# Kernel optimization log

Hardware: AMD Instinct MI355X
Metric: run time of the kernel (lower is better)

## Reference

```python
import jax, jax.numpy as jnp
import numpy as np

N_SPLIT = 4      # n_splits=[4]
RED_FC = 32      # reduce_fc
OUT_NC = 32      # reduce_adc
K = 3            # adc kernel
FMN1, FMN2 = 2048, 2048


def _adaptive_avg_matrix(in_size, out_size):
    # PyTorch AdaptiveAvgPool2d window rule: start=floor(i*in/out), end=ceil((i+1)*in/out)
    M = np.zeros((out_size, in_size), np.float32)
    for i in range(out_size):
        s = (i * in_size) // out_size
        e = -((-(i + 1) * in_size) // out_size)
        M[i, s:e] = 1.0 / (e - s)
    return jnp.asarray(M)


def grid_slice(x, n_split):
    # x: (B,C,H,W); H,W divisible by n_split (xh_padding==0). Pad 1, take overlapping tiles.
    B, C, H, W = x.shape
    hs, ws = H // n_split, W // n_split
    xp = jnp.pad(x, ((0, 0), (0, 0), (1, 1), (1, 1)))
    tiles = [xp[:, :, i * hs:i * hs + hs + 2, j * ws:j * ws + ws + 2]
             for i in range(n_split) for j in range(n_split)]
    return jnp.stack(tiles, axis=1)  # (B, n^2, C, hs+2, ws+2)


def grid_splice(x, n_split):
    # x: (B, n^2, C, hs, ws) tiles in row-major (hh, ww) order -> (B, C, H, W)
    B, T, C, hs, ws = x.shape
    x = x.reshape(B, n_split, n_split, C, hs, ws)
    x = x.transpose(0, 3, 1, 4, 2, 5)
    return x.reshape(B, C, n_split * hs, n_split * ws)


def conv2d(x, w, b, padding):
    y = jax.lax.conv_general_dilated(x, w, (1, 1), padding,
                                     dimension_numbers=("NCHW", "OIHW", "NCHW"))
    return y + b[None, :, None, None]


def setup_inputs() -> dict:
    key = jax.random.key(0)
    ks = jax.random.split(key, 8)
    B, C, H, W = 4, 64, 256, 256
    fc_size = RED_FC * RED_FC                    # 1024
    wsize = OUT_NC * C * K * K                   # 18432
    f32 = jnp.float32
    return {
        "feature": jax.random.normal(ks[0], (B, C, H, W), f32),
        # reducer: Conv(C->C,3,p1) + LeakyReLU(0.2) + Conv(C->1,3,p1) + Tanh
        "rw1": jax.random.normal(ks[1], (C, C, 3, 3), f32) * 0.05,
        "rb1": jnp.zeros((C,), f32),
        "rw2": jax.random.normal(ks[2], (1, C, 3, 3), f32) * 0.05,
        "rb2": jnp.zeros((1,), f32),
        # filter-manifold network: fc_size -> 2048 -> 2048 -> (weights + bias)
        "fw1": jax.random.normal(ks[3], (fc_size, FMN1), f32) * 0.02,
        "fb1": jnp.zeros((FMN1,), f32),
        "fw2": jax.random.normal(ks[4], (FMN1, FMN2), f32) * 0.02,
        "fb2": jnp.zeros((FMN2,), f32),
        "fw3": jax.random.normal(ks[5], (FMN2, wsize + OUT_NC), f32) * 0.01,
        "fb3": jnp.zeros((wsize + OUT_NC,), f32),
    }


def reference(feature, rw1, rb1, rw2, rb2, fw1, fb1, fw2, fb2, fw3, fb3):
    B, C, H, W = feature.shape
    # reducer -> 1-channel adaptive map
    h = conv2d(feature, rw1, rb1, ((1, 1), (1, 1)))
    h = jnp.where(h >= 0, h, 0.2 * h)                       # LeakyReLU(0.2)
    adaptive = jnp.tanh(conv2d(h, rw2, rb2, ((1, 1), (1, 1))))  # (B,1,H,W)

    # per-region context gram via adaptive avg pool to (32,32)
    adap = grid_slice(adaptive, N_SPLIT)                    # (B,T,1,hs+2,ws+2)
    Bt, T, ac, ah, aw = adap.shape
    Mh = _adaptive_avg_matrix(ah, RED_FC)
    Mw = _adaptive_avg_matrix(aw, RED_FC)
    gram = jnp.einsum("ph,btchw,qw->btcpq", Mh, adap, Mw).reshape(B * T, -1)  # (B*T,1024)

    # FMN generates per-(batch,tile) conv weights + bias
    g = jax.nn.relu(gram @ fw1 + fb1)
    g = jax.nn.relu(g @ fw2 + fb2)
    wb = g @ fw3 + fb3                                      # (B*T, wsize+OUT_NC)
    wsize = OUT_NC * C * K * K
    dyn_w = wb[:, :wsize].reshape(B * T * OUT_NC, C, K, K)
    dyn_b = wb[:, wsize:]                                   # (B*T, OUT_NC)

    # dynamic-weight VALID conv per tile via grouped conv
    fea = grid_slice(feature, N_SPLIT)                      # (B,T,C,hs+2,ws+2)
    fh, fw_ = fea.shape[-2], fea.shape[-1]
    x = fea.reshape(1, B * T * C, fh, fw_)
    y = jax.lax.conv_general_dilated(x, dyn_w, (1, 1), "VALID",
                                     dimension_numbers=("NCHW", "OIHW", "NCHW"),
                                     feature_group_count=B * T)
    y = y.reshape(B * T, OUT_NC, fh - 2, fw_ - 2) + dyn_b[:, :, None, None]
    y = grid_splice(y.reshape(B, T, OUT_NC, fh - 2, fw_ - 2), N_SPLIT)  # (B,32,H,W)

    # short_cut=True, training path: concat along channels
    return jnp.concatenate([feature, y], axis=1)            # (B, C+32, H, W)
```

## Files before the change

### kernel.cpp

```cpp
#include <hip/hip_runtime.h>


__global__ __launch_bounds__(256) void transp_rw1_k(
    const float* __restrict__ rw1, float* __restrict__ rt)
{
    int idx = blockIdx.x * 256 + threadIdx.x;
    if (idx >= 36864) return;
    int ocg = idx / 9216;
    int r   = idx - ocg * 9216;
    int ic  = r / 144;
    int r2  = r - ic * 144;
    int k   = r2 >> 4;
    int o   = r2 & 15;
    rt[idx] = rw1[(((size_t)(ocg * 16 + o) * 64 + ic) * 9) + k];
}

template <int MODE>
__global__ __launch_bounds__(256, 3) void conv3x3_v2(
    const float* __restrict__ in,
    const float* __restrict__ wt,
    const float* __restrict__ bbf,
    float* __restrict__ outb)
{
    __shared__ float sIn[8 * 34 * 36];

    const int bx = blockIdx.x, by = blockIdx.y, bz = blockIdx.z;
    int b, ocg;
    if (MODE == 0) { b = bz >> 2; ocg = bz & 3; }
    else           { b = bz >> 1; ocg = bz & 1; }
    const int tid = threadIdx.x;
    const int tx = tid & 15, ty = tid >> 4;
    const int x0 = bx * 32, y0 = by * 32;

    int bt = 0;
    const float* wbase;
    if (MODE == 0) {
        wbase = wt + ocg * 9216;
    } else {
        bt = b * 16 + (by >> 1) * 4 + (bx >> 1);
        wbase = wt + (size_t)bt * 18464 + ocg * 9216;
    }

    float acc[2][2][16];
#pragma unroll
    for (int rg = 0; rg < 2; ++rg)
#pragma unroll
        for (int p = 0; p < 2; ++p)
#pragma unroll
            for (int oc = 0; oc < 16; ++oc) acc[rg][p][oc] = 0.f;

    for (int cc = 0; cc < 8; ++cc) {
        __syncthreads();
        for (int idx = tid; idx < 8 * 34 * 34; idx += 256) {
            int ic  = idx / 1156;
            int rem = idx - ic * 1156;
            int r   = rem / 34;
            int c   = rem - r * 34;
            int gy = y0 + r - 1, gx = x0 + c - 1;
            float v = 0.f;
            if ((unsigned)gy < 256u && (unsigned)gx < 256u)
                v = in[(((size_t)b * 64 + cc * 8 + ic) * 256 + gy) * 256 + gx];
            sIn[ic * 1224 + r * 36 + c] = v;
        }
        __syncthreads();

        const float* wc = wbase + cc * 8 * 144;
        for (int ic = 0; ic < 8; ++ic) {
            const float* sI = &sIn[ic * 1224 + ty * 36 + 2 * tx];
            const float* wp = wc + ic * 144;
#pragma unroll
            for (int kh = 0; kh < 3; ++kh) {
                float w[3][16];
#pragma unroll
                for (int kw = 0; kw < 3; ++kw) {
                    *(float4*)&w[kw][0]  = *(const float4*)&wp[(kh * 3 + kw) * 16 + 0];
                    *(float4*)&w[kw][4]  = *(const float4*)&wp[(kh * 3 + kw) * 16 + 4];
                    *(float4*)&w[kw][8]  = *(const float4*)&wp[(kh * 3 + kw) * 16 + 8];
                    *(float4*)&w[kw][12] = *(const float4*)&wp[(kh * 3 + kw) * 16 + 12];
                }
#pragma unroll
                for (int rg = 0; rg < 2; ++rg) {
                    const float* rp = sI + (rg * 16 + kh) * 36;
                    float2 a  = *(const float2*)&rp[0];
                    float2 bq = *(const float2*)&rp[2];
                    float iv[4] = {a.x, a.y, bq.x, bq.y};
#pragma unroll
                    for (int kw = 0; kw < 3; ++kw) {
#pragma unroll
                        for (int oc = 0; oc < 16; ++oc) {
                            acc[rg][0][oc] += iv[kw]     * w[kw][oc];
                            acc[rg][1][oc] += iv[kw + 1] * w[kw][oc];
                        }
                    }
                }
            }
        }
    }

#pragma unroll
    for (int rg = 0; rg < 2; ++rg) {
        const int gy = y0 + ty + rg * 16;
#pragma unroll
        for (int oc = 0; oc < 16; ++oc) {
            float bv;
            int plane;
            if (MODE == 0) {
                bv = bbf[ocg * 16 + oc];
                plane = b * 96 + ocg * 16 + oc;
            } else {
                bv = bbf[(size_t)bt * 18464 + 18432 + ocg * 16 + oc];
                plane = b * 96 + 64 + ocg * 16 + oc;
            }
            float v0 = acc[rg][0][oc] + bv;
            float v1 = acc[rg][1][oc] + bv;
            if (MODE == 0) {
                v0 = (v0 >= 0.f) ? v0 : 0.2f * v0;
                v1 = (v1 >= 0.f) ? v1 : 0.2f * v1;
            }
            size_t o = (((size_t)plane) * 256 + gy) * 256 + x0 + 2 * tx;
            float2 st = {v0, v1};
            *(float2*)&outb[o] = st;
        }
    }
}

__global__ __launch_bounds__(256) void conv2_tanh_k(
    const float* __restrict__ hin,
    const float* __restrict__ rw2,
    const float* __restrict__ rb2,
    float* __restrict__ ad)
{
    __shared__ float sIn[16 * 18 * 35];
    __shared__ float sW[144];
    const int bx = blockIdx.x, by = blockIdx.y, b = blockIdx.z;
    const int tid = threadIdx.x;
    const int tx = tid & 15, ty = tid >> 4;
    const int x0 = bx * 32, y0 = by * 16;
    float a0 = 0.f, a1 = 0.f;

    for (int cc = 0; cc < 4; ++cc) {
        __syncthreads();
        for (int idx = tid; idx < 16 * 18 * 34; idx += 256) {
            int ic = idx / 612;
            int rem = idx - ic * 612;
            int row = rem / 34;
            int col = rem - row * 34;
            int gy = y0 + row - 1, gx = x0 + col - 1;
            float v = 0.f;
            if ((unsigned)gy < 256u && (unsigned)gx < 256u)
                v = hin[(((size_t)b * 96 + cc * 16 + ic) * 256 + gy) * 256 + gx];
            sIn[ic * 630 + row * 35 + col] = v;
        }
        if (tid < 144) sW[tid] = rw2[cc * 144 + tid];
        __syncthreads();

        for (int ic = 0; ic < 16; ++ic) {
            const float* sI = &sIn[ic * 630 + ty * 35 + tx];
            const float* sWi = &sW[ic * 9];
#pragma unroll
            for (int k = 0; k < 9; ++k) {
                const int kh = k / 3, kw = k - kh * 3;
                float w = sWi[k];
                a0 += sI[kh * 35 + kw] * w;
                a1 += sI[kh * 35 + kw + 16] * w;
            }
        }
    }
    float bias = rb2[0];
    size_t o = ((size_t)b * 256 + y0 + ty) * 256 + x0 + tx;
    ad[o] = tanhf(a0 + bias);
    ad[o + 16] = tanhf(a1 + bias);
}

__global__ __launch_bounds__(256) void gram_pool_k(
    const float* __restrict__ adaptive, float* __restrict__ gram)
{
    int idx = blockIdx.x * 256 + threadIdx.x;
    int bt = idx >> 10;
    int pq = idx & 1023;
    int p = pq >> 5, q = pq & 31;
    int b = bt >> 4, t = bt & 15;
    int ti = t >> 2, tj = t & 3;
    int sp = (p * 33) >> 4, ep = ((p + 1) * 33 + 15) >> 4;
    int sq = (q * 33) >> 4, eq = ((q + 1) * 33 + 15) >> 4;
    float s = 0.f;
    for (int hh = sp; hh < ep; ++hh) {
        int gy = ti * 64 + hh - 1;
        if ((unsigned)gy >= 256u) continue;
        for (int w = sq; w < eq; ++w) {
            int gx = tj * 64 + w - 1;
            if ((unsigned)gx < 256u) s += adaptive[((size_t)b * 256 + gy) * 256 + gx];
        }
    }
    gram[idx] = s / (float)((ep - sp) * (eq - sq));
}

__global__ __launch_bounds__(256) void fc_gemm_k(
    const float* __restrict__ A, const float* __restrict__ Bm,
    const float* __restrict__ bias, float* __restrict__ Cm,
    int K, int N, int act, int trans)
{
    __shared__ float As[16][68];
    __shared__ float Bs[16][64];
    const int n0 = blockIdx.x * 64;
    const int tid = threadIdx.x;
    const int tx = tid & 15, ty = tid >> 4;
    float acc[4][4];
#pragma unroll
    for (int i = 0; i < 4; ++i)
#pragma unroll
        for (int j = 0; j < 4; ++j) acc[i][j] = 0.f;

    const int mA = tid >> 2, kA = (tid & 3) * 4;
    const int kB = tid >> 4, nB = (tid & 15) * 4;

    for (int k0 = 0; k0 < K; k0 += 16) {
        __syncthreads();
        float4 av = *(const float4*)&A[(size_t)mA * K + k0 + kA];
        As[kA + 0][mA] = av.x;
        As[kA + 1][mA] = av.y;
        As[kA + 2][mA] = av.z;
        As[kA + 3][mA] = av.w;
        {
            int gn = n0 + nB;
            const float* bp = Bm + (size_t)(k0 + kB) * N + gn;
            float b0 = 0.f, b1 = 0.f, b2 = 0.f, b3 = 0.f;
            if (gn + 3 < N) {
                float4 u = *(const float4*)bp;
                b0 = u.x; b1 = u.y; b2 = u.z; b3 = u.w;
            } else {
                if (gn < N)     b0 = bp[0];
                if (gn + 1 < N) b1 = bp[1];
                if (gn + 2 < N) b2 = bp[2];
            }
            Bs[kB][nB + 0] = b0; Bs[kB][nB + 1] = b1;
            Bs[kB][nB + 2] = b2; Bs[kB][nB + 3] = b3;
        }
        __syncthreads();
#pragma unroll
        for (int kk = 0; kk < 16; ++kk) {
            float4 a = *(const float4*)&As[kk][ty * 4];
            float4 bb = *(const float4*)&Bs[kk][tx * 4];
            acc[0][0] += a.x * bb.x; acc[0][1] += a.x * bb.y; acc[0][2] += a.x * bb.z; acc[0][3] += a.x * bb.w;
            acc[1][0] += a.y * bb.x; acc[1][1] += a.y * bb.y; acc[1][2] += a.y * bb.z; acc[1][3] += a.y * bb.w;
            acc[2][0] += a.z * bb.x; acc[2][1] += a.z * bb.y; acc[2][2] += a.z * bb.z; acc[2][3] += a.z * bb.w;
            acc[3][0] += a.w * bb.x; acc[3][1] += a.w * bb.y; acc[3][2] += a.w * bb.z; acc[3][3] += a.w * bb.w;
        }
    }
#pragma unroll
    for (int i = 0; i < 4; ++i) {
        int m = ty * 4 + i;
#pragma unroll
        for (int j = 0; j < 4; ++j) {
            int n = n0 + tx * 4 + j;
            if (n < N) {
                float v = acc[i][j] + bias[n];
                if (act) v = fmaxf(v, 0.f);
                int col = n;
                if (trans && n < 18432) {
                    int oc  = n / 576;
                    int rem = n - oc * 576;
                    col = (oc >> 4) * 9216 + rem * 16 + (oc & 15);
                }
                Cm[(size_t)m * N + col] = v;
            }
        }
    }
}

__global__ __launch_bounds__(256) void copy_feat_k(
    const float4* __restrict__ f, float4* __restrict__ o)
{
    int idx = blockIdx.x * 256 + threadIdx.x;
    int plane = idx >> 14;
    int off = idx & 16383;
    int b = plane >> 6, c = plane & 63;
    o[((size_t)(b * 96 + c)) * 16384 + off] = f[idx];
}

extern "C" void kernel_launch(void* const* d_in, const int* in_sizes, int n_in,
                              void* d_out, int out_size, void* d_ws, size_t ws_size,
                              hipStream_t stream) {
    const float* feature = (const float*)d_in[0];
    const float* rw1 = (const float*)d_in[1];
    const float* rb1 = (const float*)d_in[2];
    const float* rw2 = (const float*)d_in[3];
    const float* rb2 = (const float*)d_in[4];
    const float* fw1 = (const float*)d_in[5];
    const float* fb1 = (const float*)d_in[6];
    const float* fw2 = (const float*)d_in[7];
    const float* fb2 = (const float*)d_in[8];
    const float* fw3 = (const float*)d_in[9];
    const float* fb3 = (const float*)d_in[10];
    float* out = (float*)d_out;

    float* adaptive = (float*)d_ws;
    float* gram = adaptive + 262144;
    float* g1 = gram + 65536;
    float* g2 = g1 + 131072;
    float* wb = g2 + 131072;
    float* rw1t = g1;

    transp_rw1_k<<<dim3(144), 256, 0, stream>>>(rw1, rw1t);
    conv3x3_v2<0><<<dim3(8, 8, 16), 256, 0, stream>>>(feature, rw1t, rb1, out);
    conv2_tanh_k<<<dim3(8, 16, 4), 256, 0, stream>>>(out, rw2, rb2, adaptive);
    gram_pool_k<<<dim3(256), 256, 0, stream>>>(adaptive, gram);
    fc_gemm_k<<<dim3(32), 256, 0, stream>>>(gram, fw1, fb1, g1, 1024, 2048, 1, 0);
    fc_gemm_k<<<dim3(32), 256, 0, stream>>>(g1, fw2, fb2, g2, 2048, 2048, 1, 0);
    fc_gemm_k<<<dim3(289), 256, 0, stream>>>(g2, fw3, fb3, wb, 2048, 18464, 0, 1);
    conv3x3_v2<1><<<dim3(8, 8, 8), 256, 0, stream>>>(feature, wb, wb, out);
    copy_feat_k<<<dim3(16384), 256, 0, stream>>>((const float4*)feature, (float4*)out);
}
```

Before: 1.302 ms.

## Retile 3x3 convs to 32 output channels per thread; stream FC weights directly

The 3x3 conv kernels now have each thread compute 32 output channels for one row pair instead of 16 channels for two rows. This halves the spatial tile height, shrinking shared memory, and raises the occupancy hint to 4 blocks. Input tiles get reused across more output channels, with fewer halo reloads per FLOP, at the cost of more accumulator registers. The FC GEMM drops its shared-memory B tile and reads weights straight from global memory with float4 loads, and several accumulations use explicit fmaf.

```diff
diff --git a/kernel.cpp b/kernel.cpp
--- a/kernel.cpp
+++ b/kernel.cpp
@@ -16,80 +16,77 @@
 }
 
 template <int MODE>
-__global__ __launch_bounds__(256, 3) void conv3x3_v2(
+__global__ __launch_bounds__(256, 4) void conv3x3_v3(
     const float* __restrict__ in,
     const float* __restrict__ wt,
     const float* __restrict__ bbf,
     float* __restrict__ outb)
 {
-    __shared__ float sIn[8 * 34 * 36];
+    __shared__ float sIn[8 * 18 * 36];
 
     const int bx = blockIdx.x, by = blockIdx.y, bz = blockIdx.z;
     int b, ocg;
-    if (MODE == 0) { b = bz >> 2; ocg = bz & 3; }
-    else           { b = bz >> 1; ocg = bz & 1; }
+    if (MODE == 0) { b = bz >> 1; ocg = bz & 1; }
+    else           { b = bz;      ocg = 0;      }
     const int tid = threadIdx.x;
     const int tx = tid & 15, ty = tid >> 4;
-    const int x0 = bx * 32, y0 = by * 32;
+    const int x0 = bx * 32, y0 = by * 16;
 
     int bt = 0;
     const float* wbase;
     if (MODE == 0) {
-        wbase = wt + ocg * 9216;
+        wbase = wt + (size_t)ocg * 2 * 9216;
     } else {
-        bt = b * 16 + (by >> 1) * 4 + (bx >> 1);
-        wbase = wt + (size_t)bt * 18464 + ocg * 9216;
-    }
-
-    float acc[2][2][16];
-#pragma unroll
-    for (int rg = 0; rg < 2; ++rg)
-#pragma unroll
-        for (int p = 0; p < 2; ++p)
-#pragma unroll
-            for (int oc = 0; oc < 16; ++oc) acc[rg][p][oc] = 0.f;
+        bt = b * 16 + (by >> 2) * 4 + (bx >> 1);
+        wbase = wt + (size_t)bt * 18464;
+    }
+
+    float acc[2][32];
+#pragma unroll
+    for (int p = 0; p < 2; ++p)
+#pragma unroll
+        for (int oc = 0; oc < 32; ++oc) acc[p][oc] = 0.f;
 
     for (int cc = 0; cc < 8; ++cc) {
         __syncthreads();
-        for (int idx = tid; idx < 8 * 34 * 34; idx += 256) {
-            int ic  = idx / 1156;
-            int rem = idx - ic * 1156;
+        for (int idx = tid; idx < 8 * 18 * 34; idx += 256) {
+            int ic  = idx / 612;
+            int rem = idx - ic * 612;
             int r   = rem / 34;
             int c   = rem - r * 34;
             int gy = y0 + r - 1, gx = x0 + c - 1;
             float v = 0.f;
             if ((unsigned)gy < 256u && (unsigned)gx < 256u)
                 v = in[(((size_t)b * 64 + cc * 8 + ic) * 256 + gy) * 256 + gx];
-            sIn[ic * 1224 + r * 36 + c] = v;
-        }
-        __syncthreads();
-
-        const float* wc = wbase + cc * 8 * 144;
+            sIn[ic * 648 + r * 36 + c] = v;
+        }
+        __syncthreads();
+
         for (int ic = 0; ic < 8; ++ic) {
-            const float* sI = &sIn[ic * 1224 + ty * 36 + 2 * tx];
-            const float* wp = wc + ic * 144;
+            const float* sI = &sIn[ic * 648 + ty * 36 + 2 * tx];
 #pragma unroll
             for (int kh = 0; kh < 3; ++kh) {
-                float w[3][16];
-#pragma unroll
-                for (int kw = 0; kw < 3; ++kw) {
-                    *(float4*)&w[kw][0]  = *(const float4*)&wp[(kh * 3 + kw) * 16 + 0];
-                    *(float4*)&w[kw][4]  = *(const float4*)&wp[(kh * 3 + kw) * 16 + 4];
-                    *(float4*)&w[kw][8]  = *(const float4*)&wp[(kh * 3 + kw) * 16 + 8];
-                    *(float4*)&w[kw][12] = *(const float4*)&wp[(kh * 3 + kw) * 16 + 12];
-                }
-#pragma unroll
-                for (int rg = 0; rg < 2; ++rg) {
-                    const float* rp = sI + (rg * 16 + kh) * 36;
-                    float2 a  = *(const float2*)&rp[0];
-                    float2 bq = *(const float2*)&rp[2];
-                    float iv[4] = {a.x, a.y, bq.x, bq.y};
+                const float* rp = sI + kh * 36;
+                float2 pa = *(const float2*)&rp[0];
+                float2 pb = *(const float2*)&rp[2];
+                float i0 = pa.x, i1 = pa.y, i2 = pb.x, i3 = pb.y;
+#pragma unroll
+                for (int oh = 0; oh < 2; ++oh) {
+                    const float* wp = wbase + (size_t)oh * 9216
+                                    + (cc * 8 + ic) * 144 + kh * 48;
 #pragma unroll
                     for (int kw = 0; kw < 3; ++kw) {
-#pragma unroll
-                        for (int oc = 0; oc < 16; ++oc) {
-                            acc[rg][0][oc] += iv[kw]     * w[kw][oc];
-                            acc[rg][1][oc] += iv[kw + 1] * w[kw][oc];
+                        float w[16];
+                        *(float4*)&w[0]  = *(const float4*)&wp[kw * 16 + 0];
+                        *(float4*)&w[4]  = *(const float4*)&wp[kw * 16 + 4];
+                        *(float4*)&w[8]  = *(const float4*)&wp[kw * 16 + 8];
+                        *(float4*)&w[12] = *(const float4*)&wp[kw * 16 + 12];
+                        float ia = (kw == 0) ? i0 : (kw == 1) ? i1 : i2;
+                        float ib = (kw == 0) ? i1 : (kw == 1) ? i2 : i3;
+#pragma unroll
+                        for (int o = 0; o < 16; ++o) {
+                            acc[0][oh * 16 + o] = fmaf(ia, w[o], acc[0][oh * 16 + o]);
+                            acc[1][oh * 16 + o] = fmaf(ib, w[o], acc[1][oh * 16 + o]);
                         }
                     }
                 }
@@ -97,30 +94,27 @@
         }
     }
 
-#pragma unroll
-    for (int rg = 0; rg < 2; ++rg) {
-        const int gy = y0 + ty + rg * 16;
-#pragma unroll
-        for (int oc = 0; oc < 16; ++oc) {
-            float bv;
-            int plane;
-            if (MODE == 0) {
-                bv = bbf[ocg * 16 + oc];
-                plane = b * 96 + ocg * 16 + oc;
-            } else {
-                bv = bbf[(size_t)bt * 18464 + 18432 + ocg * 16 + oc];
-                plane = b * 96 + 64 + ocg * 16 + oc;
-            }
-            float v0 = acc[rg][0][oc] + bv;
-            float v1 = acc[rg][1][oc] + bv;
-            if (MODE == 0) {
-                v0 = (v0 >= 0.f) ? v0 : 0.2f * v0;
-                v1 = (v1 >= 0.f) ? v1 : 0.2f * v1;
-            }
-            size_t o = (((size_t)plane) * 256 + gy) * 256 + x0 + 2 * tx;
-            float2 st = {v0, v1};
-            *(float2*)&outb[o] = st;
-        }
+    const int gy = y0 + ty;
+#pragma unroll
+    for (int oc = 0; oc < 32; ++oc) {
+        float bv;
+        int plane;
+        if (MODE == 0) {
+            bv = bbf[ocg * 32 + oc];
+            plane = b * 96 + ocg * 32 + oc;
+        } else {
+            bv = bbf[(size_t)bt * 18464 + 18432 + oc];
+            plane = b * 96 + 64 + oc;
+        }
+        float v0 = acc[0][oc] + bv;
+        float v1 = acc[1][oc] + bv;
+        if (MODE == 0) {
+            v0 = (v0 >= 0.f) ? v0 : 0.2f * v0;
+            v1 = (v1 >= 0.f) ? v1 : 0.2f * v1;
+        }
+        size_t o = (((size_t)plane) * 256 + gy) * 256 + x0 + 2 * tx;
+        float2 st = {v0, v1};
+        *(float2*)&outb[o] = st;
     }
 }
 
@@ -161,8 +155,8 @@
             for (int k = 0; k < 9; ++k) {
                 const int kh = k / 3, kw = k - kh * 3;
                 float w = sWi[k];
-                a0 += sI[kh * 35 + kw] * w;
-                a1 += sI[kh * 35 + kw + 16] * w;
+                a0 = fmaf(sI[kh * 35 + kw], w, a0);
+                a1 = fmaf(sI[kh * 35 + kw + 16], w, a1);
             }
         }
     }
@@ -201,7 +195,6 @@
     int K, int N, int act, int trans)
 {
     __shared__ float As[16][68];
-    __shared__ float Bs[16][64];
     const int n0 = blockIdx.x * 64;
     const int tid = threadIdx.x;
     const int tx = tid & 15, ty = tid >> 4;
@@ -212,7 +205,9 @@
         for (int j = 0; j < 4; ++j) acc[i][j] = 0.f;
 
     const int mA = tid >> 2, kA = (tid & 3) * 4;
-    const int kB = tid >> 4, nB = (tid & 15) * 4;
+
+    const int gnb = n0 + tx * 4;
+    const float* bp = Bm + (gnb + 3 < N ? gnb : 0);
 
     for (int k0 = 0; k0 < K; k0 += 16) {
         __syncthreads();
@@ -221,30 +216,20 @@
         As[kA + 1][mA] = av.y;
         As[kA + 2][mA] = av.z;
         As[kA + 3][mA] = av.w;
-        {
-            int gn = n0 + nB;
-            const float* bp = Bm + (size_t)(k0 + kB) * N + gn;
-            float b0 = 0.f, b1 = 0.f, b2 = 0.f, b3 = 0.f;
-            if (gn + 3 < N) {
-                float4 u = *(const float4*)bp;
-                b0 = u.x; b1 = u.y; b2 = u.z; b3 = u.w;
-            } else {
-                if (gn < N)     b0 = bp[0];
-                if (gn + 1 < N) b1 = bp[1];
-                if (gn + 2 < N) b2 = bp[2];
-            }
-            Bs[kB][nB + 0] = b0; Bs[kB][nB + 1] = b1;
-            Bs[kB][nB + 2] = b2; Bs[kB][nB + 3] = b3;
-        }
         __syncthreads();
 #pragma unroll
         for (int kk = 0; kk < 16; ++kk) {
+            float4 bb = *(const float4*)bp;
+            bp += N;
             float4 a = *(const float4*)&As[kk][ty * 4];
-            float4 bb = *(const float4*)&Bs[kk][tx * 4];
-            acc[0][0] += a.x * bb.x; acc[0][1] += a.x * bb.y; acc[0][2] += a.x * bb.z; acc[0][3] += a.x * bb.w;
-            acc[1][0] += a.y * bb.x; acc[1][1] += a.y * bb.y; acc[1][2] += a.y * bb.z; acc[1][3] += a.y * bb.w;
-            acc[2][0] += a.z * bb.x; acc[2][1] += a.z * bb.y; acc[2][2] += a.z * bb.z; acc[2][3] += a.z * bb.w;
-            acc[3][0] += a.w * bb.x; acc[3][1] += a.w * bb.y; acc[3][2] += a.w * bb.z; acc[3][3] += a.w * bb.w;
+            acc[0][0] = fmaf(a.x, bb.x, acc[0][0]); acc[0][1] = fmaf(a.x, bb.y, acc[0][1]);
+            acc[0][2] = fmaf(a.x, bb.z, acc[0][2]); acc[0][3] = fmaf(a.x, bb.w, acc[0][3]);
+            acc[1][0] = fmaf(a.y, bb.x, acc[1][0]); acc[1][1] = fmaf(a.y, bb.y, acc[1][1]);
+            acc[1][2] = fmaf(a.y, bb.z, acc[1][2]); acc[1][3] = fmaf(a.y, bb.w, acc[1][3]);
+            acc[2][0] = fmaf(a.z, bb.x, acc[2][0]); acc[2][1] = fmaf(a.z, bb.y, acc[2][1]);
+            acc[2][2] = fmaf(a.z, bb.z, acc[2][2]); acc[2][3] = fmaf(a.z, bb.w, acc[2][3]);
+            acc[3][0] = fmaf(a.w, bb.x, acc[3][0]); acc[3][1] = fmaf(a.w, bb.y, acc[3][1]);
+            acc[3][2] = fmaf(a.w, bb.z, acc[3][2]); acc[3][3] = fmaf(a.w, bb.w, acc[3][3]);
         }
     }
 #pragma unroll
@@ -302,12 +287,12 @@
     float* rw1t = g1;
 
     transp_rw1_k<<<dim3(144), 256, 0, stream>>>(rw1, rw1t);
-    conv3x3_v2<0><<<dim3(8, 8, 16), 256, 0, stream>>>(feature, rw1t, rb1, out);
+    conv3x3_v3<0><<<dim3(8, 16, 8), 256, 0, stream>>>(feature, rw1t, rb1, out);
     conv2_tanh_k<<<dim3(8, 16, 4), 256, 0, stream>>>(out, rw2, rb2, adaptive);
     gram_pool_k<<<dim3(256), 256, 0, stream>>>(adaptive, gram);
     fc_gemm_k<<<dim3(32), 256, 0, stream>>>(gram, fw1, fb1, g1, 1024, 2048, 1, 0);
     fc_gemm_k<<<dim3(32), 256, 0, stream>>>(g1, fw2, fb2, g2, 2048, 2048, 1, 0);
     fc_gemm_k<<<dim3(289), 256, 0, stream>>>(g2, fw3, fb3, wb, 2048, 18464, 0, 1);
-    conv3x3_v2<1><<<dim3(8, 8, 8), 256, 0, stream>>>(feature, wb, wb, out);
+    conv3x3_v3<1><<<dim3(8, 16, 4), 256, 0, stream>>>(feature, wb, wb, out);
     copy_feat_k<<<dim3(16384), 256, 0, stream>>>((const float4*)feature, (float4*)out);
 }
```

New measurement: 2.104 ms. 1.62x slower.
